# Performance work log

Hardware: AMD Instinct MI355X
Metric: run time of the kernel (lower is better)

The kernel has to match this reference:

```python
import jax, jax.numpy as jnp
import numpy as np

N = 50000      # nodes
E = 250000     # edges
IN = 256       # in_channels
OUT = 256      # out_channels
H = 4          # heads
C = OUT // H   # per-head channels = 64
MSG = 128
TIME = 64
ED = MSG + TIME + 2   # edge_dim = 194


def _glorot(k, shape):
    return (jax.random.normal(k, shape, jnp.float32) / np.sqrt(shape[0])).astype(jnp.float32)


def setup_inputs() -> dict:
    ks = jax.random.split(jax.random.key(0), 16)
    z = lambda: jnp.zeros((H * C,), jnp.float32)
    inp = {
        "x": jax.random.normal(ks[0], (N, IN), jnp.float32),
        "edge_index": jax.random.randint(ks[1], (2, E), 0, N),
        "edge_attr": jax.random.normal(ks[2], (E, ED), jnp.float32),
        # conv1 params (in_channels=IN)
        "Wq1": _glorot(ks[3], (IN, H * C)), "bq1": z(),
        "Wk1": _glorot(ks[4], (IN, H * C)), "bk1": z(),
        "Wv1": _glorot(ks[5], (IN, H * C)), "bv1": z(),
        "We1": _glorot(ks[6], (ED, H * C)),              # lin_edge has no bias in PyG
        "Ws1": _glorot(ks[7], (IN, H * C)), "bs1": z(),  # skip/root connection
        # conv2 params (in_channels=OUT)
        "Wq2": _glorot(ks[8], (OUT, H * C)), "bq2": z(),
        "Wk2": _glorot(ks[9], (OUT, H * C)), "bk2": z(),
        "Wv2": _glorot(ks[10], (OUT, H * C)), "bv2": z(),
        "We2": _glorot(ks[11], (ED, H * C)),
        "Ws2": _glorot(ks[12], (OUT, H * C)), "bs2": z(),
    }
    return inp


def _tconv(x, src, dst, edge_attr, Wq, bq, Wk, bk, Wv, bv, We, Ws, bs):
    """PyG TransformerConv (heads=H, concat=True, root_weight=True), eval mode."""
    n = x.shape[0]
    q = (x @ Wq + bq).reshape(n, H, C)
    k = (x @ Wk + bk).reshape(n, H, C)
    v = (x @ Wv + bv).reshape(n, H, C)
    e = (edge_attr @ We).reshape(-1, H, C)          # [E,H,C]
    kj = k[src] + e                                  # key + edge embedding
    vj = v[src] + e                                  # value + edge embedding
    logits = jnp.einsum('ehc,ehc->eh', q[dst], kj) / np.sqrt(C)  # [E,H]
    # segment softmax over incoming edges of each dst node
    m = jax.lax.stop_gradient(jax.ops.segment_max(logits, dst, num_segments=n))
    ex = jnp.exp(logits - m[dst])
    denom = jax.ops.segment_sum(ex, dst, num_segments=n)
    a = ex / (denom[dst] + 1e-16)                    # [E,H]
    agg = jax.ops.segment_sum(vj * a[:, :, None], dst, num_segments=n)  # [N,H,C]
    return agg.reshape(n, H * C) + x @ Ws + bs


def reference(x, edge_index, edge_attr,
              Wq1, bq1, Wk1, bk1, Wv1, bv1, We1, Ws1, bs1,
              Wq2, bq2, Wk2, bk2, Wv2, bv2, We2, Ws2, bs2):
    src, dst = edge_index[0], edge_index[1]
    h = jax.nn.relu(_tconv(x, src, dst, edge_attr,
                           Wq1, bq1, Wk1, bk1, Wv1, bv1, We1, Ws1, bs1))
    # dropout is identity in eval mode
    return _tconv(h, src, dst, edge_attr,
                  Wq2, bq2, Wk2, bk2, Wv2, bv2, We2, Ws2, bs2)
```

## Files before the change

### kernel.cpp

```cpp
#include <hip/hip_runtime.h>

#define N_NODES 50000
#define N_EDGES 250000
#define DIM 256
#define ED 194
#define EDP 224
#define MP_NODE 50048
#define MP_EDGE 250112

typedef __bf16 bf16x8 __attribute__((ext_vector_type(8)));
typedef float f32x4 __attribute__((ext_vector_type(4)));
typedef short s16x8 __attribute__((ext_vector_type(8)));
typedef short s16x4 __attribute__((ext_vector_type(4)));
typedef unsigned short u16x8 __attribute__((ext_vector_type(8)));

__device__ __forceinline__ float bf2f(unsigned short b){
  union { unsigned int u; float f; } v; v.u = ((unsigned int)b)<<16; return v.f;
}
__device__ __forceinline__ short f2bf(float f){
  union { float f; unsigned int u; } v; v.f = f;
  unsigned int u = v.u;
  return (short)((u + 0x7fffu + ((u>>16)&1u))>>16);
}

__device__ __forceinline__ void gload_lds16(const void* g, void* l){
  __builtin_amdgcn_global_load_lds(
      (const __attribute__((address_space(1))) unsigned int*)g,
      (__attribute__((address_space(3))) unsigned int*)l, 16, 0, 0);
}

__global__ __launch_bounds__(256) void convert_x_kernel(
    const float* __restrict__ x, short* __restrict__ xb, int* __restrict__ deg)
{
  int idx = blockIdx.x*256 + threadIdx.x;
  if (idx < N_NODES) deg[idx] = 0;
  s16x4 o;
  if (idx < N_NODES*64){
    float4 a = *(const float4*)(x + (size_t)idx*4);
    o[0]=f2bf(a.x); o[1]=f2bf(a.y); o[2]=f2bf(a.z); o[3]=f2bf(a.w);
  } else {
    o[0]=0; o[1]=0; o[2]=0; o[3]=0;
  }
  *(s16x4*)(xb + (size_t)idx*4) = o;
}

#define E_ROWS 32
__global__ __launch_bounds__(256) void convert_e_kernel(
    const float* __restrict__ ea, short* __restrict__ eb)
{
  __shared__ float lds[E_ROWS*ED];
  int row0 = blockIdx.x * E_ROWS;
  int tid = threadIdx.x;
  int base = row0 * ED;
  int valid = N_EDGES*ED - base;

  for (int i = tid; i < E_ROWS*ED/4; i += 256){
    float4 v;
    if (i*4 < valid) v = *(const float4*)(ea + base + i*4);
    else             v = make_float4(0.f,0.f,0.f,0.f);
    *(float4*)(lds + i*4) = v;
  }
  __syncthreads();

  for (int u = tid; u < E_ROWS*28; u += 256){
    int row = u / 28;
    int c8  = u - row*28;
    int col = c8*8;
    s16x8 o;
    if (col + 8 <= ED){
      #pragma unroll
      for (int j2=0;j2<4;j2++){
        float2 f = *(const float2*)(lds + row*ED + col + j2*2);
        o[j2*2]   = f2bf(f.x);
        o[j2*2+1] = f2bf(f.y);
      }
    } else {
      #pragma unroll
      for (int j=0;j<8;j++){
        int c = col + j;
        o[j] = (c < ED) ? f2bf(lds[row*ED + c]) : (short)0;
      }
    }
    *(s16x8*)(eb + (size_t)(row0+row)*EDP + col) = o;
  }
}

__global__ __launch_bounds__(256) void prep_weights(
    const float* __restrict__ Wq, const float* __restrict__ Wk,
    const float* __restrict__ Wv, const float* __restrict__ Ws,
    const float* __restrict__ We,
    const float* __restrict__ b0, const float* __restrict__ b1,
    const float* __restrict__ b2, const float* __restrict__ b3,
    short* __restrict__ WtN, short* __restrict__ WtE, float* __restrict__ biasN)
{
  __shared__ short lds[64*65];
  int b = blockIdx.x, tid = threadIdx.x;
  if (b < 64){
    int mat = b>>4, tile = b&15;
    int i0 = (tile>>2)*64, o0 = (tile&3)*64;
    const float* W = (mat==0)?Wq:((mat==1)?Wk:((mat==2)?Wv:Ws));
    #pragma unroll
    for (int t=0;t<16;t++){
      int idx = t*256+tid; int r = idx>>6, c = idx&63;
      lds[r*65+c] = f2bf(W[(size_t)(i0+r)*256 + o0 + c]);
    }
    __syncthreads();
    #pragma unroll
    for (int t=0;t<4;t++){
      int idx = t*256+tid; int r = idx>>4, c4 = (idx&15)*4;
      s16x4 o;
      o[0]=lds[(c4+0)*65+r]; o[1]=lds[(c4+1)*65+r];
      o[2]=lds[(c4+2)*65+r]; o[3]=lds[(c4+3)*65+r];
      *(s16x4*)(WtN + (mat<<16) + (o0+r)*256 + i0 + c4) = o;
    }
  } else if (b < 80){
    int b2 = b-64;
    int k0 = (b2>>2)*64, o0 = (b2&3)*64;
    #pragma unroll
    for (int t=0;t<16;t++){
      int idx = t*256+tid; int r = idx>>6, c = idx&63;
      int k = k0+r;
      lds[r*65+c] = (k<ED) ? f2bf(We[(size_t)k*256 + o0 + c]) : (short)0;
    }
    __syncthreads();
    #pragma unroll
    for (int t=0;t<4;t++){
      int idx = t*256+tid; int r = idx>>4, c4 = (idx&15)*4;
      if (k0 + c4 < EDP){
        s16x4 o;
        o[0]=lds[(c4+0)*65+r]; o[1]=lds[(c4+1)*65+r];
        o[2]=lds[(c4+2)*65+r]; o[3]=lds[(c4+3)*65+r];
        *(s16x4*)(WtE + (o0+r)*EDP + k0 + c4) = o;
      }
    }
  } else {
    for (int t = tid; t < 1024; t += 256){
      const float* bb = (t<256)?b0:((t<512)?b1:((t<768)?b2:b3));
      biasN[t] = bb[t&255];
    }
  }
}

__global__ __launch_bounds__(256) void count_deg(const int* __restrict__ dst, int* __restrict__ deg){
  int e = blockIdx.x*256 + threadIdx.x;
  if (e < N_EDGES) atomicAdd(&deg[dst[e]], 1);
}
#define SCAN_NBLK 196
__global__ __launch_bounds__(256) void scan_p1(const int* __restrict__ deg, int* __restrict__ part){
  int t = threadIdx.x;
  int i = blockIdx.x*256 + t;
  int v = (i<N_NODES)? deg[i] : 0;
  #pragma unroll
  for (int off=32; off; off>>=1) v += __shfl_xor(v, off, 64);
  __shared__ int s[4];
  if ((t&63)==0) s[t>>6] = v;
  __syncthreads();
  if (t==0) part[blockIdx.x] = s[0]+s[1]+s[2]+s[3];
}
__global__ __launch_bounds__(256) void scan_p2(int* __restrict__ part){
  __shared__ int s[256];
  int t = threadIdx.x;
  int v = (t<SCAN_NBLK)? part[t] : 0;
  s[t] = v; __syncthreads();
  for (int off=1; off<256; off<<=1){
    int x = (t>=off)? s[t-off] : 0;
    __syncthreads();
    s[t] += x;
    __syncthreads();
  }
  part[t] = (t==0)? 0 : s[t-1];
}
__global__ __launch_bounds__(256) void scan_p3(const int* __restrict__ deg,
    const int* __restrict__ part, int* __restrict__ rowptr, int* __restrict__ cursor){
  __shared__ int s[256];
  int t = threadIdx.x;
  int i = blockIdx.x*256 + t;
  int v = (i<N_NODES)? deg[i] : 0;
  s[t] = v; __syncthreads();
  for (int off=1; off<256; off<<=1){
    int x = (t>=off)? s[t-off] : 0;
    __syncthreads();
    s[t] += x;
    __syncthreads();
  }
  if (i < N_NODES){ rowptr[i+1] = part[blockIdx.x] + s[t]; cursor[i] = 0; }
  if (i == 0) rowptr[0] = 0;
}
__global__ __launch_bounds__(256) void scatter_edges(
    const int* __restrict__ src, const int* __restrict__ dst,
    const int* __restrict__ rowptr, int* __restrict__ cursor, int2* __restrict__ csr)
{
  int e = blockIdx.x*256 + threadIdx.x;
  if (e < N_EDGES){
    int d = dst[e];
    int pos = atomicAdd(&cursor[d], 1);
    csr[rowptr[d] + pos] = make_int2(src[e]<<11, e<<9);
  }
}

template<int K, int NLD, bool HAS_BIAS>
__global__ __launch_bounds__(256) void gemm_bt(
    const short* __restrict__ A, const short* __restrict__ Bt,
    const float* __restrict__ bias, short* __restrict__ out, int M)
{
  __shared__ short As[128*32];
  __shared__ short Bs[128*32];
  int tid = threadIdx.x;
  int lane = tid & 63, wave = tid >> 6;
  int m0 = blockIdx.x*128, n0 = blockIdx.y*128;

  int srow = tid>>2, scol = (tid&3)*8;
  const short* gA = A + (size_t)(m0+srow)*K + scol;
  const short* gB = Bt + (size_t)(n0+srow)*K + scol;
  short* ldsA1 = As + wave*512;
  short* ldsA2 = As + 2048 + wave*512;
  short* ldsB1 = Bs + wave*512;
  short* ldsB2 = Bs + 2048 + wave*512;

  int wr = wave>>1, wc = wave&1;
  int fr = lane & 15;
  int kq = lane >> 4;
  f32x4 acc[4][4];
  #pragma unroll
  for (int a=0;a<4;a++)
    #pragma unroll
    for (int b=0;b<4;b++) acc[a][b] = (f32x4){0.f,0.f,0.f,0.f};

  for (int k0=0; k0<K; k0+=32){
    __syncthreads();
    gload_lds16(gA + k0,                ldsA1);
    gload_lds16(gA + (size_t)64*K + k0, ldsA2);
    gload_lds16(gB + k0,                ldsB1);
    gload_lds16(gB + (size_t)64*K + k0, ldsB2);
    __syncthreads();

    bf16x8 af[4], bf[4];
    const short* ar = As + (wr*64 + fr)*32 + kq*8;
    const short* br = Bs + (wc*64 + fr)*32 + kq*8;
    #pragma unroll
    for (int fm=0;fm<4;fm++) af[fm] = *(const bf16x8*)(ar + fm*512);
    #pragma unroll
    for (int fn=0;fn<4;fn++) bf[fn] = *(const bf16x8*)(br + fn*512);
    #pragma unroll
    for (int fm=0;fm<4;fm++)
      #pragma unroll
      for (int fn=0;fn<4;fn++)
        acc[fm][fn] = __builtin_amdgcn_mfma_f32_16x16x32_bf16(af[fm], bf[fn], acc[fm][fn], 0, 0, 0);
  }

  int cr = (lane>>4)*4;
  int cc = lane & 15;
  #pragma unroll
  for (int fm=0;fm<4;fm++){
    #pragma unroll
    for (int fn=0;fn<4;fn++){
      int col = n0 + wc*64 + fn*16 + cc;
      float bv = HAS_BIAS ? bias[col] : 0.f;
      #pragma unroll
      for (int i=0;i<4;i++){
        int row = m0 + wr*64 + fm*16 + cr + i;
        if (row < M) out[(size_t)row*NLD + col] = f2bf(acc[fm][fn][i] + bv);
      }
    }
  }
}

__global__ __launch_bounds__(256) void edge_phase_kernel(
    const short* __restrict__ QKVS, const short* __restrict__ Eemb,
    const int* __restrict__ rowptr, const int2* __restrict__ csr,
    short* __restrict__ out_bf, float* __restrict__ out_f, int relu)
{
  int tid = threadIdx.x, wave = tid>>6, lane = tid&63;
  int node = blockIdx.x*4 + wave;
  if (node >= N_NODES){
    if (node < MP_NODE && out_bf){
      s16x4 z; z[0]=0; z[1]=0; z[2]=0; z[3]=0;
      *(s16x4*)(out_bf + (size_t)node*256 + lane*4) = z;
    }
    return;
  }
  int half = lane>>5;
  int hl   = lane&31;
  int c8   = hl*8;
  const unsigned short* base = (const unsigned short*)QKVS + (size_t)node*1024;

  u16x8 qu = *(const u16x8*)(base + c8);
  float q[8];
  #pragma unroll
  for (int j=0;j<8;j++) q[j] = bf2f(qu[j])*0.125f;

  int beg = rowptr[node], end = rowptr[node+1];
  float l = 0.f;
  float a[8];
  #pragma unroll
  for (int j=0;j<8;j++) a[j] = 0.f;
  int kb = 512 + hl*16;
  int ebo = hl*16;

  for (int idx = beg; idx < end; idx += 2){
    int j = idx + half;
    int jc = (j < end) ? j : (end-1);
    int2 se = csr[jc];
    const char* Kp = (const char*)QKVS + (unsigned)(se.x + kb);
    const char* Ep = (const char*)Eemb + (unsigned)(se.y + ebo);
    u16x8 ku = *(const u16x8*)Kp;
    u16x8 vu = *(const u16x8*)(Kp + 512);
    u16x8 eu = *(const u16x8*)Ep;
    float vv[8];
    float t = 0.f;
    #pragma unroll
    for (int c=0;c<8;c++){
      float ef = bf2f(eu[c]);
      float kf = bf2f(ku[c]) + ef;
      vv[c]    = bf2f(vu[c]) + ef;
      t += q[c]*kf;
    }
    t += __shfl_xor(t, 1, 64);
    t += __shfl_xor(t, 2, 64);
    t += __shfl_xor(t, 4, 64);
    float p = (j < end) ? __expf(t) : 0.f;
    l += p;
    #pragma unroll
    for (int c=0;c<8;c++) a[c] += p*vv[c];
  }

  l += __shfl_xor(l, 32, 64);
  #pragma unroll
  for (int c=0;c<8;c++) a[c] += __shfl_xor(a[c], 32, 64);

  float inv = (l > 0.f) ? 1.0f/l : 0.f;
  u16x8 su = *(const u16x8*)(base + 768 + c8);
  float r[8];
  #pragma unroll
  for (int c=0;c<8;c++){
    float v = a[c]*inv + bf2f(su[c]);
    r[c] = relu ? fmaxf(v, 0.f) : v;
  }

  if (out_bf){
    if (!half){
      s16x8 o;
      #pragma unroll
      for (int c=0;c<8;c++) o[c] = f2bf(r[c]);
      *(s16x8*)(out_bf + (size_t)node*256 + c8) = o;
    }
  } else {
    float4 st = half ? make_float4(r[4],r[5],r[6],r[7])
                     : make_float4(r[0],r[1],r[2],r[3]);
    *(float4*)(out_f + (size_t)node*256 + c8 + half*4) = st;
  }
}

extern "C" void kernel_launch(void* const* d_in, const int* in_sizes, int n_in,
                              void* d_out, int out_size, void* d_ws, size_t ws_size,
                              hipStream_t stream)
{
  const float* x     = (const float*)d_in[0];
  const int*   eidx  = (const int*)d_in[1];
  const float* eattr = (const float*)d_in[2];
  const float* Wq1=(const float*)d_in[3],  *bq1=(const float*)d_in[4];
  const float* Wk1=(const float*)d_in[5],  *bk1=(const float*)d_in[6];
  const float* Wv1=(const float*)d_in[7],  *bv1=(const float*)d_in[8];
  const float* We1=(const float*)d_in[9];
  const float* Ws1=(const float*)d_in[10], *bs1=(const float*)d_in[11];
  const float* Wq2=(const float*)d_in[12], *bq2=(const float*)d_in[13];
  const float* Wk2=(const float*)d_in[14], *bk2=(const float*)d_in[15];
  const float* Wv2=(const float*)d_in[16], *bv2=(const float*)d_in[17];
  const float* We2=(const float*)d_in[18];
  const float* Ws2=(const float*)d_in[19], *bs2=(const float*)d_in[20];

  char* ws = (char*)d_ws;
  size_t off = 0;
  auto alloc = [&](size_t bytes)->char*{
    char* p = ws + off; off = (off + bytes + 255) & ~(size_t)255; return p;
  };
  short* QKVS  = (short*)alloc((size_t)N_NODES*1024*2);
  short* Eemb  = (short*)alloc((size_t)N_EDGES*256*2);
  short* x_bf  = (short*)alloc((size_t)MP_NODE*DIM*2);
  short* h_bf  = (short*)alloc((size_t)MP_NODE*DIM*2);
  short* e_bf  = (short*)alloc((size_t)MP_EDGE*EDP*2);
  short* WtN   = (short*)alloc((size_t)4*65536*2);
  short* WtE   = (short*)alloc((size_t)256*EDP*2);
  float* biasN = (float*)alloc((size_t)1024*4);
  int*   deg   = (int*)alloc((size_t)N_NODES*4);
  int*   rowptr= (int*)alloc((size_t)(N_NODES+1)*4);
  int*   cursor= (int*)alloc((size_t)N_NODES*4);
  int*   part  = (int*)alloc((size_t)256*4);
  int2*  csr   = (int2*)alloc((size_t)N_EDGES*8);

  const int* srcp = eidx;
  const int* dstp = eidx + N_EDGES;

  const int EB = (N_EDGES + 255)/256;

  convert_x_kernel<<<MP_NODE*64/256,256,0,stream>>>(x, x_bf, deg);
  convert_e_kernel<<<MP_EDGE/E_ROWS,256,0,stream>>>(eattr, e_bf);

  count_deg<<<EB,256,0,stream>>>(dstp, deg);
  scan_p1<<<SCAN_NBLK,256,0,stream>>>(deg, part);
  scan_p2<<<1,256,0,stream>>>(part);
  scan_p3<<<SCAN_NBLK,256,0,stream>>>(deg, part, rowptr, cursor);
  scatter_edges<<<EB,256,0,stream>>>(srcp, dstp, rowptr, cursor, csr);

  prep_weights<<<81,256,0,stream>>>(Wq1,Wk1,Wv1,Ws1,We1,bq1,bk1,bv1,bs1,WtN,WtE,biasN);
  gemm_bt<DIM,1024,true><<<dim3(MP_NODE/128,8),256,0,stream>>>(x_bf, WtN, biasN, QKVS, N_NODES);
  gemm_bt<EDP,256,false><<<dim3(MP_EDGE/128,2),256,0,stream>>>(e_bf, WtE, nullptr, Eemb, N_EDGES);
  edge_phase_kernel<<<MP_NODE/4,256,0,stream>>>(QKVS,Eemb,rowptr,csr,h_bf,nullptr,1);

  prep_weights<<<81,256,0,stream>>>(Wq2,Wk2,Wv2,Ws2,We2,bq2,bk2,bv2,bs2,WtN,WtE,biasN);
  gemm_bt<DIM,1024,true><<<dim3(MP_NODE/128,8),256,0,stream>>>(h_bf, WtN, biasN, QKVS, N_NODES);
  gemm_bt<EDP,256,false><<<dim3(MP_EDGE/128,2),256,0,stream>>>(e_bf, WtE, nullptr, Eemb, N_EDGES);
  edge_phase_kernel<<<N_NODES/4,256,0,stream>>>(QKVS,Eemb,rowptr,csr,nullptr,(float*)d_out,0);
}
```

Before: 877.6 us.

## Compute both layers' edge embeddings in one GEMM and prefetch CSR entries

Weight preparation for both convolutions is merged into one kernel, and the two edge-embedding GEMMs become a single GEMM producing 512 columns per edge (We1 and We2 stacked). This reads edge_attr once instead of twice and removes two launches, but the Eemb buffer doubles in size and each edge row stride grows to 1024 bytes, which spreads the per-edge gathers further apart. The edge-phase loop also prefetches the next CSR entry one iteration ahead to hide the index-load latency.

```diff
diff --git a/kernel.cpp b/kernel.cpp
--- a/kernel.cpp
+++ b/kernel.cpp
@@ -85,20 +85,29 @@
   }
 }
 
-__global__ __launch_bounds__(256) void prep_weights(
-    const float* __restrict__ Wq, const float* __restrict__ Wk,
-    const float* __restrict__ Wv, const float* __restrict__ Ws,
-    const float* __restrict__ We,
-    const float* __restrict__ b0, const float* __restrict__ b1,
-    const float* __restrict__ b2, const float* __restrict__ b3,
-    short* __restrict__ WtN, short* __restrict__ WtE, float* __restrict__ biasN)
+__global__ __launch_bounds__(256) void prep_weights_all(
+    const float* __restrict__ Wq1, const float* __restrict__ Wk1,
+    const float* __restrict__ Wv1, const float* __restrict__ Ws1,
+    const float* __restrict__ We1,
+    const float* __restrict__ bq1, const float* __restrict__ bk1,
+    const float* __restrict__ bv1, const float* __restrict__ bs1,
+    const float* __restrict__ Wq2, const float* __restrict__ Wk2,
+    const float* __restrict__ Wv2, const float* __restrict__ Ws2,
+    const float* __restrict__ We2,
+    const float* __restrict__ bq2, const float* __restrict__ bk2,
+    const float* __restrict__ bv2, const float* __restrict__ bs2,
+    short* __restrict__ WtN1, short* __restrict__ WtN2,
+    short* __restrict__ WtE, float* __restrict__ biasN1, float* __restrict__ biasN2)
 {
   __shared__ short lds[64*65];
   int b = blockIdx.x, tid = threadIdx.x;
-  if (b < 64){
-    int mat = b>>4, tile = b&15;
+  if (b < 128){
+    int conv = b>>6, bb = b&63;
+    int mat = bb>>4, tile = bb&15;
     int i0 = (tile>>2)*64, o0 = (tile&3)*64;
-    const float* W = (mat==0)?Wq:((mat==1)?Wk:((mat==2)?Wv:Ws));
+    const float* W = conv ? ((mat==0)?Wq2:((mat==1)?Wk2:((mat==2)?Wv2:Ws2)))
+                          : ((mat==0)?Wq1:((mat==1)?Wk1:((mat==2)?Wv1:Ws1)));
+    short* WtN = conv ? WtN2 : WtN1;
     #pragma unroll
     for (int t=0;t<16;t++){
       int idx = t*256+tid; int r = idx>>6, c = idx&63;
@@ -113,14 +122,16 @@
       o[2]=lds[(c4+2)*65+r]; o[3]=lds[(c4+3)*65+r];
       *(s16x4*)(WtN + (mat<<16) + (o0+r)*256 + i0 + c4) = o;
     }
-  } else if (b < 80){
-    int b2 = b-64;
-    int k0 = (b2>>2)*64, o0 = (b2&3)*64;
+  } else if (b < 160){
+    int b2 = b-128;
+    int k0 = (b2>>3)*64, o0 = (b2&7)*64;
+    const float* We = (o0 < 256) ? We1 : We2;
+    int oc = o0 & 255;
     #pragma unroll
     for (int t=0;t<16;t++){
       int idx = t*256+tid; int r = idx>>6, c = idx&63;
       int k = k0+r;
-      lds[r*65+c] = (k<ED) ? f2bf(We[(size_t)k*256 + o0 + c]) : (short)0;
+      lds[r*65+c] = (k<ED) ? f2bf(We[(size_t)k*256 + oc + c]) : (short)0;
     }
     __syncthreads();
     #pragma unroll
@@ -130,12 +141,15 @@
         s16x4 o;
         o[0]=lds[(c4+0)*65+r]; o[1]=lds[(c4+1)*65+r];
         o[2]=lds[(c4+2)*65+r]; o[3]=lds[(c4+3)*65+r];
-        *(s16x4*)(WtE + (o0+r)*EDP + k0 + c4) = o;
+        *(s16x4*)(WtE + (size_t)(o0+r)*EDP + k0 + c4) = o;
       }
     }
   } else {
+    int conv = b - 160;
+    float* biasN = conv ? biasN2 : biasN1;
     for (int t = tid; t < 1024; t += 256){
-      const float* bb = (t<256)?b0:((t<512)?b1:((t<768)?b2:b3));
+      const float* bb = conv ? ((t<256)?bq2:((t<512)?bk2:((t<768)?bv2:bs2)))
+                             : ((t<256)?bq1:((t<512)?bk1:((t<768)?bv1:bs1)));
       biasN[t] = bb[t&255];
     }
   }
@@ -194,7 +208,7 @@
   if (e < N_EDGES){
     int d = dst[e];
     int pos = atomicAdd(&cursor[d], 1);
-    csr[rowptr[d] + pos] = make_int2(src[e]<<11, e<<9);
+    csr[rowptr[d] + pos] = make_int2(src[e]<<11, e<<10);
   }
 }
 
@@ -297,31 +311,36 @@
   int kb = 512 + hl*16;
   int ebo = hl*16;
 
-  for (int idx = beg; idx < end; idx += 2){
-    int j = idx + half;
-    int jc = (j < end) ? j : (end-1);
-    int2 se = csr[jc];
-    const char* Kp = (const char*)QKVS + (unsigned)(se.x + kb);
-    const char* Ep = (const char*)Eemb + (unsigned)(se.y + ebo);
-    u16x8 ku = *(const u16x8*)Kp;
-    u16x8 vu = *(const u16x8*)(Kp + 512);
-    u16x8 eu = *(const u16x8*)Ep;
-    float vv[8];
-    float t = 0.f;
-    #pragma unroll
-    for (int c=0;c<8;c++){
-      float ef = bf2f(eu[c]);
-      float kf = bf2f(ku[c]) + ef;
-      vv[c]    = bf2f(vu[c]) + ef;
-      t += q[c]*kf;
-    }
-    t += __shfl_xor(t, 1, 64);
-    t += __shfl_xor(t, 2, 64);
-    t += __shfl_xor(t, 4, 64);
-    float p = (j < end) ? __expf(t) : 0.f;
-    l += p;
-    #pragma unroll
-    for (int c=0;c<8;c++) a[c] += p*vv[c];
+  if (beg < end){
+    int j0 = beg + half;
+    int2 se = csr[(j0 < end) ? j0 : (end-1)];
+    for (int idx = beg; idx < end; idx += 2){
+      int jn = idx + 2 + half;
+      int2 se_n = csr[(jn < end) ? jn : (end-1)];
+      int j = idx + half;
+      const char* Kp = (const char*)QKVS + (unsigned)(se.x + kb);
+      const char* Ep = (const char*)Eemb + (unsigned)(se.y + ebo);
+      u16x8 ku = *(const u16x8*)Kp;
+      u16x8 vu = *(const u16x8*)(Kp + 512);
+      u16x8 eu = *(const u16x8*)Ep;
+      float vv[8];
+      float t = 0.f;
+      #pragma unroll
+      for (int c=0;c<8;c++){
+        float ef = bf2f(eu[c]);
+        float kf = bf2f(ku[c]) + ef;
+        vv[c]    = bf2f(vu[c]) + ef;
+        t += q[c]*kf;
+      }
+      t += __shfl_xor(t, 1, 64);
+      t += __shfl_xor(t, 2, 64);
+      t += __shfl_xor(t, 4, 64);
+      float p = (j < end) ? __expf(t) : 0.f;
+      l += p;
+      #pragma unroll
+      for (int c=0;c<8;c++) a[c] += p*vv[c];
+      se = se_n;
+    }
   }
 
   l += __shfl_xor(l, 32, 64);
@@ -375,13 +394,15 @@
     char* p = ws + off; off = (off + bytes + 255) & ~(size_t)255; return p;
   };
   short* QKVS  = (short*)alloc((size_t)N_NODES*1024*2);
-  short* Eemb  = (short*)alloc((size_t)N_EDGES*256*2);
+  short* Eemb  = (short*)alloc((size_t)MP_EDGE*512*2);
   short* x_bf  = (short*)alloc((size_t)MP_NODE*DIM*2);
   short* h_bf  = (short*)alloc((size_t)MP_NODE*DIM*2);
   short* e_bf  = (short*)alloc((size_t)MP_EDGE*EDP*2);
-  short* WtN   = (short*)alloc((size_t)4*65536*2);
-  short* WtE   = (short*)alloc((size_t)256*EDP*2);
-  float* biasN = (float*)alloc((size_t)1024*4);
+  short* WtN1  = (short*)alloc((size_t)4*65536*2);
+  short* WtN2  = (short*)alloc((size_t)4*65536*2);
+  short* WtE   = (short*)alloc((size_t)512*EDP*2);
+  float* biasN1= (float*)alloc((size_t)1024*4);
+  float* biasN2= (float*)alloc((size_t)1024*4);
   int*   deg   = (int*)alloc((size_t)N_NODES*4);
   int*   rowptr= (int*)alloc((size_t)(N_NODES+1)*4);
   int*   cursor= (int*)alloc((size_t)N_NODES*4);
@@ -402,13 +423,16 @@
   scan_p3<<<SCAN_NBLK,256,0,stream>>>(deg, part, rowptr, cursor);
   scatter_edges<<<EB,256,0,stream>>>(srcp, dstp, rowptr, cursor, csr);
 
-  prep_weights<<<81,256,0,stream>>>(Wq1,Wk1,Wv1,Ws1,We1,bq1,bk1,bv1,bs1,WtN,WtE,biasN);
-  gemm_bt<DIM,1024,true><<<dim3(MP_NODE/128,8),256,0,stream>>>(x_bf, WtN, biasN, QKVS, N_NODES);
-  gemm_bt<EDP,256,false><<<dim3(MP_EDGE/128,2),256,0,stream>>>(e_bf, WtE, nullptr, Eemb, N_EDGES);
+  prep_weights_all<<<162,256,0,stream>>>(
+      Wq1,Wk1,Wv1,Ws1,We1,bq1,bk1,bv1,bs1,
+      Wq2,Wk2,Wv2,Ws2,We2,bq2,bk2,bv2,bs2,
+      WtN1,WtN2,WtE,biasN1,biasN2);
+
+  gemm_bt<EDP,512,false><<<dim3(MP_EDGE/128,4),256,0,stream>>>(e_bf, WtE, nullptr, Eemb, N_EDGES);
+
+  gemm_bt<DIM,1024,true><<<dim3(MP_NODE/128,8),256,0,stream>>>(x_bf, WtN1, biasN1, QKVS, N_NODES);
   edge_phase_kernel<<<MP_NODE/4,256,0,stream>>>(QKVS,Eemb,rowptr,csr,h_bf,nullptr,1);
 
-  prep_weights<<<81,256,0,stream>>>(Wq2,Wk2,Wv2,Ws2,We2,bq2,bk2,bv2,bs2,WtN,WtE,biasN);
-  gemm_bt<DIM,1024,true><<<dim3(MP_NODE/128,8),256,0,stream>>>(h_bf, WtN, biasN, QKVS, N_NODES);
-  gemm_bt<EDP,256,false><<<dim3(MP_EDGE/128,2),256,0,stream>>>(e_bf, WtE, nullptr, Eemb, N_EDGES);
-  edge_phase_kernel<<<N_NODES/4,256,0,stream>>>(QKVS,Eemb,rowptr,csr,nullptr,(float*)d_out,0);
-}
+  gemm_bt<DIM,1024,true><<<dim3(MP_NODE/128,8),256,0,stream>>>(h_bf, WtN2, biasN2, QKVS, N_NODES);
+  edge_phase_kernel<<<N_NODES/4,256,0,stream>>>(QKVS,Eemb+256,rowptr,csr,nullptr,(float*)d_out,0);
+}
```

Result: faster. 850.0 us (-3.2%).
